# Optimization experiments

Measured on AMD Instinct MI355X. Metric: run time of the kernel, lower is better.

## Reference

```python
import jax, jax.numpy as jnp
import numpy as np

B, T, E, A = 512, 64, 1024, 32
S, D, H = 30, 200, 200          # stoch, deter, hidden
SS = D + S                      # state_size = 230
MIN_STD = 0.1
UPDATE_BIAS = -1.0
W_SCALE = 0.05


def setup_inputs() -> dict:
    key = jax.random.key(0)
    ks = jax.random.split(key, 17)
    n = jax.random.normal
    return {
        "embed":       n(ks[0], (B, T, E), jnp.float32),
        "action":      n(ks[1], (B, T, A), jnp.float32),
        "context":     n(ks[2], (B, T, SS), jnp.float32),
        "noise_prior": n(ks[3], (T, B, S), jnp.float32),
        "noise_post":  n(ks[4], (T, B, S), jnp.float32),
        "w_inp":       n(ks[5], (S + SS + A, H), jnp.float32) * W_SCALE,
        "b_inp":       jnp.zeros((H,), jnp.float32),
        "w_gru":       n(ks[6], (H + D, 3 * D), jnp.float32) * W_SCALE,
        "b_gru":       jnp.zeros((3 * D,), jnp.float32),
        "w_img_out":   n(ks[7], (D, H), jnp.float32) * W_SCALE,
        "b_img_out":   jnp.zeros((H,), jnp.float32),
        "w_obs_out":   n(ks[8], (D + E, H), jnp.float32) * W_SCALE,
        "b_obs_out":   jnp.zeros((H,), jnp.float32),
        "w_ims_stat":  n(ks[9], (H, 2 * S), jnp.float32) * W_SCALE,
        "b_ims_stat":  jnp.zeros((2 * S,), jnp.float32),
        "w_obs_stat":  n(ks[10], (H, 2 * S), jnp.float32) * W_SCALE,
        "b_obs_stat":  jnp.zeros((2 * S,), jnp.float32),
    }


def _observe(embed, action, context, noise_prior, noise_post,
             w_inp, b_inp, w_gru, b_gru, w_img_out, b_img_out,
             w_obs_out, b_obs_out, w_ims_stat, b_ims_stat,
             w_obs_stat, b_obs_stat):
    # time-major
    emb_t = jnp.swapaxes(embed, 0, 1)    # [T,B,E]
    act_t = jnp.swapaxes(action, 0, 1)   # [T,B,A]
    ctx_t = jnp.swapaxes(context, 0, 1)  # [T,B,SS]

    def step(carry, xs):
        stoch, deter = carry
        ctx, act, emb, n_p, n_o = xs
        # img_step: input MLP + GRU cell
        x = jnp.concatenate([stoch, ctx, act], -1)
        x = jax.nn.elu(x @ w_inp + b_inp)
        parts = jnp.concatenate([x, deter], -1) @ w_gru + b_gru
        reset, cand, update = jnp.split(parts, 3, -1)
        reset = jax.nn.sigmoid(reset)
        cand = jnp.tanh(reset * cand)
        update = jax.nn.sigmoid(update + UPDATE_BIAS)
        deter_new = update * cand + (1.0 - update) * deter
        # prior stats
        h = jax.nn.elu(deter_new @ w_img_out + b_img_out)
        st = h @ w_ims_stat + b_ims_stat
        pm, ps = jnp.split(st, 2, -1)
        ps = jax.nn.softplus(ps) + MIN_STD
        p_stoch = pm + ps * n_p
        # posterior stats
        ho = jax.nn.elu(jnp.concatenate([deter_new, emb], -1) @ w_obs_out + b_obs_out)
        so = ho @ w_obs_stat + b_obs_stat
        om, os_ = jnp.split(so, 2, -1)
        os_ = jax.nn.softplus(os_) + MIN_STD
        o_stoch = om + os_ * n_o
        out = jnp.concatenate([om, os_, o_stoch, pm, ps, p_stoch, deter_new], -1)
        return (o_stoch, deter_new), out

    carry0 = (jnp.zeros((B, S), embed.dtype), jnp.zeros((B, D), embed.dtype))
    _, ys = jax.lax.scan(step, carry0, (ctx_t, act_t, emb_t, noise_prior, noise_post))
    # ys: [T,B,6S+D] -> [B,T,6S+D]  (post mean/std/stoch, prior mean/std/stoch, deter)
    return jnp.swapaxes(ys, 0, 1)


def reference(embed, action, context, noise_prior, noise_post,
              w_inp, b_inp, w_gru, b_gru, w_img_out, b_img_out,
              w_obs_out, b_obs_out, w_ims_stat, b_ims_stat,
              w_obs_stat, b_obs_stat):
    return _observe(embed, action, context, noise_prior, noise_post,
                    w_inp, b_inp, w_gru, b_gru, w_img_out, b_img_out,
                    w_obs_out, b_obs_out, w_ims_stat, b_ims_stat,
                    w_obs_stat, b_obs_stat)
```

## Files before the change

### kernel.cpp

```cpp
#include <hip/hip_runtime.h>
#include <cstddef>

typedef short short8 __attribute__((ext_vector_type(8)));
typedef float f32x4 __attribute__((ext_vector_type(4)));
typedef unsigned short u16;

#define Bn 512
#define Tn 64
#define En 1024
#define An 32
#define Sn 30
#define Dn 200
#define SSn 230
#define OUTC 380

#define U16_WINP0  0
#define U16_WINPCA 6656
#define U16_WGRU   66560
#define U16_WIMG   326144
#define U16_WOBSD  372736
#define U16_WIMS   419328
#define U16_WOBSS  433664
#define U16_WOBSE  448000
#define U16_PREO   660992
#define U16_PREI   7214592

#define WINP0_8  0
#define WINPCA_8 832
#define WGRU_8   8320
#define WIMG_8   40768
#define WOBSD_8  46592
#define WIMS_8   52416
#define WOBSS_8  54208
#define WOBSE_8  56000

#define DEV static __device__ __forceinline__
#define MFMA(a,b,c) __builtin_amdgcn_mfma_f32_16x16x32_bf16((a),(b),(c),0,0,0)

DEV u16 f2bf(float f) {
  union { float f; unsigned u; } v; v.f = f;
  return (u16)((v.u + 0x7FFFu + ((v.u >> 16) & 1u)) >> 16);
}
DEV float bf2f(u16 h) {
  union { unsigned u; float f; } v; v.u = ((unsigned)h) << 16; return v.f;
}
DEV float fexp(float x)  { return __builtin_amdgcn_exp2f(x * 1.44269504f); }
DEV float sigm(float x)  { return __builtin_amdgcn_rcpf(1.f + fexp(-x)); }
DEV float tanhf_(float x){ return 1.f - 2.f * __builtin_amdgcn_rcpf(fexp(2.f * x) + 1.f); }
DEV float elu1(float x)  { return x > 0.f ? x : fexp(x) - 1.f; }
DEV float splus(float x) { return 0.69314718f * __builtin_amdgcn_logf(1.f + fexp(x)); }

DEV void barx() {
  asm volatile("s_waitcnt lgkmcnt(0)" ::: "memory");
  __builtin_amdgcn_s_barrier();
  asm volatile("" ::: "memory");
}

__global__ __launch_bounds__(256) void k_pack2(
    const float* __restrict__ w_inp, const float* __restrict__ w_gru,
    const float* __restrict__ w_img, const float* __restrict__ w_obs,
    const float* __restrict__ w_ims, const float* __restrict__ w_obss,
    u16* __restrict__ ws) {
  int s = blockIdx.x;
  const float* src; int KT, Kr, ldN, roff, colbase, cmax; size_t dstbase; int ntKT;
  if (s < 13)      { src=w_inp;  KT=1;  Kr=30;   ldN=200; roff=0;   int nt=s;    colbase=nt*16; cmax=min(16,200-colbase); dstbase=U16_WINP0;  ntKT=nt*KT; }
  else if (s < 26) { src=w_inp;  KT=9;  Kr=262;  ldN=200; roff=30;  int nt=s-13; colbase=nt*16; cmax=min(16,200-colbase); dstbase=U16_WINPCA; ntKT=nt*KT; }
  else if (s < 65) { src=w_gru;  KT=13; Kr=400;  ldN=600; roff=0;   int ntp=s-26; int g=ntp/3, p=ntp%3;
                     colbase=p*200+g*16; cmax=min(16,200-g*16); dstbase=U16_WGRU; ntKT=ntp*KT; }
  else if (s < 78) { src=w_img;  KT=7;  Kr=200;  ldN=200; roff=0;   int nt=s-65; colbase=nt*16; cmax=min(16,200-colbase); dstbase=U16_WIMG;  ntKT=nt*KT; }
  else if (s < 91) { src=w_obs;  KT=7;  Kr=200;  ldN=200; roff=0;   int nt=s-78; colbase=nt*16; cmax=min(16,200-colbase); dstbase=U16_WOBSD; ntKT=nt*KT; }
  else if (s < 95) { src=w_ims;  KT=7;  Kr=200;  ldN=60;  roff=0;   int nt=s-91; colbase=nt*16; cmax=min(16,60-colbase);  dstbase=U16_WIMS;  ntKT=nt*KT; }
  else if (s < 99) { src=w_obss; KT=7;  Kr=200;  ldN=60;  roff=0;   int nt=s-95; colbase=nt*16; cmax=min(16,60-colbase);  dstbase=U16_WOBSS; ntKT=nt*KT; }
  else             { src=w_obs;  KT=32; Kr=1024; ldN=200; roff=200; int nt=s-99; colbase=nt*16; cmax=min(16,200-colbase); dstbase=U16_WOBSE; ntKT=nt*KT; }

  __shared__ float Ws[2048];
  int tid = threadIdx.x;
  int nchunk = (KT + 3) >> 2;
  for (int kc = 0; kc < nchunk; ++kc) {
    __syncthreads();
    for (int i = tid; i < 2048; i += 256) {
      int r = i >> 4, c = i & 15;
      int k = kc * 128 + r;
      Ws[i] = (k < Kr && c < cmax) ? src[(size_t)(roff + k) * ldN + colbase + c] : 0.f;
    }
    __syncthreads();
    int nf = KT - kc * 4; if (nf > 4) nf = 4;
    int fi = tid >> 6, lane = tid & 63;
    if (fi < nf) {
      int kt = kc * 4 + fi;
      union { u16 h[8]; short8 v; } pk;
#pragma unroll
      for (int j = 0; j < 8; ++j)
        pk.h[j] = f2bf(Ws[(fi * 32 + ((lane >> 4) << 3) + j) * 16 + (lane & 15)]);
      *(short8*)&ws[dstbase + (size_t)(ntKT + kt) * 512 + lane * 8] = pk.v;
    }
  }
}

__global__ __launch_bounds__(256) void k_pre(
    const float* __restrict__ emb, const float* __restrict__ ctx,
    const float* __restrict__ act, const float* __restrict__ b_obs,
    const float* __restrict__ b_inp, u16* __restrict__ ws) {
  __shared__ u16 Asm[64 * 72];
  __shared__ short8 Bsm[26 * 64];
  const short8* Wb = (const short8*)ws;
  u16* preO = ws + U16_PREO;
  u16* preI = ws + U16_PREI;

  int tid = threadIdx.x, wv = tid >> 6, lane = tid & 63;
  int lrow = lane & 15, quad = lane >> 4;
  int m0 = blockIdx.x * 64;
  int t = m0 >> 9, b0 = m0 & 511;

  const f32x4 z4 = {0.f, 0.f, 0.f, 0.f};
  f32x4 acc[13];

#pragma unroll
  for (int i = 0; i < 13; ++i) acc[i] = z4;
  for (int kc = 0; kc < 16; ++kc) {
    __syncthreads();
#pragma unroll
    for (int q = 0; q < 4; ++q) {
      int i = tid + q * 256;
      int row = i >> 4, c4 = i & 15;
      const float* src = emb + ((size_t)((b0 + row) * Tn + t)) * En + kc * 64 + c4 * 4;
      float4 v = *(const float4*)src;
      union { u16 h[4]; unsigned long long ll; } p;
      p.h[0] = f2bf(v.x); p.h[1] = f2bf(v.y); p.h[2] = f2bf(v.z); p.h[3] = f2bf(v.w);
      *(unsigned long long*)&Asm[row * 72 + c4 * 4] = p.ll;
    }
    for (int q = 0; q < 7; ++q) {
      int i = tid + q * 256;
      if (i < 1664) {
        int pair = i >> 6, l = i & 63;
        int ktl = pair / 13, nt = pair % 13;
        Bsm[i] = Wb[WOBSE_8 + (size_t)(nt * 32 + kc * 2 + ktl) * 64 + l];
      }
    }
    __syncthreads();
#pragma unroll
    for (int ktl = 0; ktl < 2; ++ktl) {
      short8 a = *(const short8*)&Asm[(wv * 16 + lrow) * 72 + ktl * 32 + quad * 8];
#pragma unroll
      for (int nt = 0; nt < 13; ++nt)
        acc[nt] = MFMA(a, Bsm[(ktl * 13 + nt) * 64 + lane], acc[nt]);
    }
  }
#pragma unroll
  for (int nt = 0; nt < 13; ++nt) {
    int col = nt * 16 + lrow;
    if (col < 200) {
      float bias = b_obs[col];
#pragma unroll
      for (int r = 0; r < 4; ++r) {
        int m = t * 512 + b0 + wv * 16 + quad * 4 + r;
        preO[(size_t)m * 200 + col] = f2bf(acc[nt][r] + bias);
      }
    }
  }

#pragma unroll
  for (int i = 0; i < 13; ++i) acc[i] = z4;
  for (int kc = 0; kc < 5; ++kc) {
    __syncthreads();
#pragma unroll
    for (int q = 0; q < 4; ++q) {
      int i = tid + q * 256;
      int row = i >> 4, c4 = i & 15;
      union { u16 h[4]; unsigned long long ll; } p;
#pragma unroll
      for (int e = 0; e < 4; ++e) {
        int k = kc * 64 + c4 * 4 + e;
        float v = 0.f;
        if (k < 230)      v = ctx[((size_t)(b0 + row) * Tn + t) * SSn + k];
        else if (k < 262) v = act[((size_t)(b0 + row) * Tn + t) * An + (k - 230)];
        p.h[e] = f2bf(v);
      }
      *(unsigned long long*)&Asm[row * 72 + c4 * 4] = p.ll;
    }
    int nktl = (kc < 4) ? 2 : 1;
    for (int q = 0; q < 7; ++q) {
      int i = tid + q * 256;
      if (i < nktl * 13 * 64) {
        int pair = i >> 6, l = i & 63;
        int ktl = pair / 13, nt = pair % 13;
        Bsm[i] = Wb[WINPCA_8 + (size_t)(nt * 9 + kc * 2 + ktl) * 64 + l];
      }
    }
    __syncthreads();
    for (int ktl = 0; ktl < nktl; ++ktl) {
      short8 a = *(const short8*)&Asm[(wv * 16 + lrow) * 72 + ktl * 32 + quad * 8];
#pragma unroll
      for (int nt = 0; nt < 13; ++nt)
        acc[nt] = MFMA(a, Bsm[(ktl * 13 + nt) * 64 + lane], acc[nt]);
    }
  }
#pragma unroll
  for (int nt = 0; nt < 13; ++nt) {
    int col = nt * 16 + lrow;
    if (col < 200) {
      float bias = b_inp[col];
#pragma unroll
      for (int r = 0; r < 4; ++r) {
        int m = t * 512 + b0 + wv * 16 + quad * 4 + r;
        preI[(size_t)m * 200 + col] = f2bf(acc[nt][r] + bias);
      }
    }
  }
}

__global__ __launch_bounds__(512, 1) void k_scan(
    const float* __restrict__ g_no, const float* __restrict__ b_gru,
    const float* __restrict__ b_obss, const u16* __restrict__ ws,
    float* __restrict__ out) {

  __shared__ u16 AB[16 * 872];
  __shared__ u16 Uin[16 * 40];
  __shared__ u16 hoA[16 * 232];
  __shared__ u16 WdL[91 * 512];

  const short8* Wb = (const short8*)ws;
  const u16* preO = ws + U16_PREO;
  const u16* preI = ws + U16_PREI;

  const int tid = threadIdx.x, wv = tid >> 6, lane = tid & 63;
  const int lrow = lane & 15, quad = lane >> 4;
  const int b0 = blockIdx.x * 16;
  const f32x4 z4 = {0.f, 0.f, 0.f, 0.f};

  const bool two = wv < 5;
  const int g1 = two ? (wv + 8) : wv;
  const int colA0 = wv * 16 + lrow;
  const int colA1 = g1 * 16 + lrow;
  const int dcol0 = colA0;
  const int dcol1 = colA1;
  const int nrow = tid / 30, ns = tid - nrow * 30;

  short8 fA0 = Wb[WINP0_8 + (size_t)wv * 64 + lane];
  short8 fA1 = Wb[WINP0_8 + (size_t)g1 * 64 + lane];

  float bgr0 = b_gru[dcol0], bgc0 = b_gru[200 + dcol0], bgu0 = b_gru[400 + dcol0] - 1.f;
  float bgr1 = 0.f, bgc1 = 0.f, bgu1 = -1.f;
  if (two && dcol1 < 200) { bgr1 = b_gru[dcol1]; bgc1 = b_gru[200 + dcol1]; bgu1 = b_gru[400 + dcol1] - 1.f; }
  const int cD = (wv & 3) * 16 + lrow;
  const float bD = (wv < 4 && cD < 60) ? b_obss[cD] : 0.f;

  const short8* pr0 = Wb + WGRU_8 + (size_t)((3 * wv + 0) * 13) * 64 + lane;
  const short8* pc0 = Wb + WGRU_8 + (size_t)((3 * wv + 1) * 13) * 64 + lane;
  const short8* pu0 = Wb + WGRU_8 + (size_t)((3 * wv + 2) * 13) * 64 + lane;
  const short8* pr1 = Wb + WGRU_8 + (size_t)((3 * g1 + 0) * 13) * 64 + lane;
  const short8* pc1 = Wb + WGRU_8 + (size_t)((3 * g1 + 1) * 13) * 64 + lane;
  const short8* pu1 = Wb + WGRU_8 + (size_t)((3 * g1 + 2) * 13) * 64 + lane;
  const short8* bpD = Wb + WOBSS_8 + (size_t)(((wv < 4) ? wv : 0) * 7) * 64 + lane;

  short8 wR0[2], wC0_[2], wU0[2], wR1[2], wC1_[2], wU1[2];
#pragma unroll
  for (int k = 0; k < 2; ++k) {
    wR0[k] = pr0[k * 64]; wC0_[k] = pc0[k * 64]; wU0[k] = pu0[k * 64];
    wR1[k] = pr1[k * 64]; wC1_[k] = pc1[k * 64]; wU1[k] = pu1[k * 64];
  }
  short8 wD[7];
#pragma unroll
  for (int k = 0; k < 7; ++k) wD[k] = bpD[k * 64];

  {
    short8* Wl = (short8*)WdL;
    for (int i = tid; i < 91 * 64; i += 512) Wl[i] = Wb[WOBSD_8 + i];
  }

  for (int i = tid; i < 16 * 872; i += 512) AB[i] = 0;
  for (int i = tid; i < 16 * 40; i += 512) Uin[i] = 0;
  for (int i = tid; i < 16 * 232; i += 512) hoA[i] = 0;
  __syncthreads();

  float* stoF = (float*)AB;

  u16 pinC0[4], pinC1[4] = {0,0,0,0}, pobC0[4], pobC1[4] = {0,0,0,0};
  float vnoC = 0.f;
  {
    size_t mb = (size_t)b0 + quad * 4;
#pragma unroll
    for (int r = 0; r < 4; ++r) pinC0[r] = preI[(mb + r) * 200 + colA0];
#pragma unroll
    for (int r = 0; r < 4; ++r) pobC0[r] = preO[(mb + r) * 200 + colA0];
    if (two && colA1 < 200) {
#pragma unroll
      for (int r = 0; r < 4; ++r) pinC1[r] = preI[(mb + r) * 200 + colA1];
#pragma unroll
      for (int r = 0; r < 4; ++r) pobC1[r] = preO[(mb + r) * 200 + colA1];
    }
    if (tid < 480) vnoC = g_no[((size_t)b0 + nrow) * Sn + ns];
  }

  for (int t = 0; t < Tn; ++t) {
    const int par = t & 1;
    const int pb = par * 424, qb = 424 - pb;
    const int qbf = qb >> 1;

    barx();

    {
      short8 aU = *(const short8*)&Uin[lrow * 40 + quad * 8];
      f32x4 a0 = MFMA(aU, fA0, z4);
#pragma unroll
      for (int r = 0; r < 4; ++r)
        AB[(quad * 4 + r) * 872 + pb + colA0] = f2bf(elu1(a0[r] + bf2f(pinC0[r])));
      if (two) {
        f32x4 a1 = MFMA(aU, fA1, z4);
        if (colA1 < 200) {
#pragma unroll
          for (int r = 0; r < 4; ++r)
            AB[(quad * 4 + r) * 872 + pb + colA1] = f2bf(elu1(a1[r] + bf2f(pinC1[r])));
        }
      }
    }

    u16 pinN0[4], pinN1[4] = {0,0,0,0}, pobN0[4], pobN1[4] = {0,0,0,0};
    float vnoN = 0.f;
    {
      int tn = (t + 1 < Tn) ? (t + 1) : t;
      size_t mb = (size_t)tn * 512 + b0 + quad * 4;
#pragma unroll
      for (int r = 0; r < 4; ++r) pinN0[r] = preI[(mb + r) * 200 + colA0];
#pragma unroll
      for (int r = 0; r < 4; ++r) pobN0[r] = preO[(mb + r) * 200 + colA0];
      if (two && colA1 < 200) {
#pragma unroll
        for (int r = 0; r < 4; ++r) pinN1[r] = preI[(mb + r) * 200 + colA1];
#pragma unroll
        for (int r = 0; r < 4; ++r) pobN1[r] = preO[(mb + r) * 200 + colA1];
      }
      if (tid < 480) vnoN = g_no[((size_t)tn * 512 + b0 + nrow) * Sn + ns];
    }

    barx();

    {
      short8 ax[13];
#pragma unroll
      for (int kt = 0; kt < 13; ++kt)
        ax[kt] = *(const short8*)&AB[lrow * 872 + pb + kt * 32 + quad * 8];
      f32x4 ar0 = z4, ac0 = z4, au0 = z4, ar1 = z4, ac1 = z4, au1 = z4;
      if (two) {
#pragma unroll
        for (int kt = 0; kt < 13; ++kt) {
          short8 br0 = (kt < 2) ? wR0[kt]  : pr0[kt * 64];
          short8 br1 = (kt < 2) ? wR1[kt]  : pr1[kt * 64];
          short8 bc0 = (kt < 2) ? wC0_[kt] : pc0[kt * 64];
          short8 bc1 = (kt < 2) ? wC1_[kt] : pc1[kt * 64];
          short8 bu0 = (kt < 2) ? wU0[kt]  : pu0[kt * 64];
          short8 bu1 = (kt < 2) ? wU1[kt]  : pu1[kt * 64];
          ar0 = MFMA(ax[kt], br0, ar0);
          ar1 = MFMA(ax[kt], br1, ar1);
          ac0 = MFMA(ax[kt], bc0, ac0);
          ac1 = MFMA(ax[kt], bc1, ac1);
          au0 = MFMA(ax[kt], bu0, au0);
          au1 = MFMA(ax[kt], bu1, au1);
        }
      } else {
#pragma unroll
        for (int kt = 0; kt < 13; ++kt) {
          short8 br0 = (kt < 2) ? wR0[kt]  : pr0[kt * 64];
          short8 bc0 = (kt < 2) ? wC0_[kt] : pc0[kt * 64];
          short8 bu0 = (kt < 2) ? wU0[kt]  : pu0[kt * 64];
          ar0 = MFMA(ax[kt], br0, ar0);
          ac0 = MFMA(ax[kt], bc0, ac0);
          au0 = MFMA(ax[kt], bu0, au0);
        }
      }
#pragma unroll
      for (int r = 0; r < 4; ++r) {
        int row = quad * 4 + r;
        float dold = bf2f(AB[row * 872 + pb + 200 + dcol0]);
        float rs = sigm(ar0[r] + bgr0);
        float cnd = tanhf_(rs * (ac0[r] + bgc0));
        float up = sigm(au0[r] + bgu0);
        float dn = up * cnd + (1.f - up) * dold;
        AB[row * 872 + qb + 200 + dcol0] = f2bf(dn);
        __builtin_nontemporal_store(dn, &out[((size_t)(b0 + row) * Tn + t) * OUTC + 180 + dcol0]);
      }
      if (two && dcol1 < 200) {
#pragma unroll
        for (int r = 0; r < 4; ++r) {
          int row = quad * 4 + r;
          float dold = bf2f(AB[row * 872 + pb + 200 + dcol1]);
          float rs = sigm(ar1[r] + bgr1);
          float cnd = tanhf_(rs * (ac1[r] + bgc1));
          float up = sigm(au1[r] + bgu1);
          float dn = up * cnd + (1.f - up) * dold;
          AB[row * 872 + qb + 200 + dcol1] = f2bf(dn);
          __builtin_nontemporal_store(dn, &out[((size_t)(b0 + row) * Tn + t) * OUTC + 180 + dcol1]);
        }
      }
    }

    barx();

    {
      short8 ad[7];
#pragma unroll
      for (int kt = 0; kt < 7; ++kt)
        ad[kt] = *(const short8*)&AB[lrow * 872 + qb + 200 + kt * 32 + quad * 8];
      f32x4 h0 = z4, h1 = z4;
      if (two) {
#pragma unroll
        for (int kt = 0; kt < 7; ++kt) {
          h0 = MFMA(ad[kt], *(const short8*)&WdL[(wv * 7 + kt) * 512 + lane * 8], h0);
          h1 = MFMA(ad[kt], *(const short8*)&WdL[(g1 * 7 + kt) * 512 + lane * 8], h1);
        }
      } else {
#pragma unroll
        for (int kt = 0; kt < 7; ++kt)
          h0 = MFMA(ad[kt], *(const short8*)&WdL[(wv * 7 + kt) * 512 + lane * 8], h0);
      }
#pragma unroll
      for (int r = 0; r < 4; ++r)
        hoA[(quad * 4 + r) * 232 + colA0] = f2bf(elu1(h0[r] + bf2f(pobC0[r])));
      if (two && colA1 < 200) {
#pragma unroll
        for (int r = 0; r < 4; ++r)
          hoA[(quad * 4 + r) * 232 + colA1] = f2bf(elu1(h1[r] + bf2f(pobC1[r])));
      }
    }

    barx();

    if (wv < 4) {
      f32x4 acc = z4;
#pragma unroll
      for (int kt = 0; kt < 7; ++kt) {
        short8 a = *(const short8*)&hoA[lrow * 232 + kt * 32 + quad * 8];
        acc = MFMA(a, wD[kt], acc);
      }
      if (cD < 60) {
#pragma unroll
        for (int r = 0; r < 4; ++r)
          stoF[(quad * 4 + r) * 436 + qbf + cD] = acc[r] + bD;
      }
    }

    barx();

    if (tid < 480) {
      size_t ob = ((size_t)(b0 + nrow) * Tn + t) * OUTC;
      float om = stoF[nrow * 436 + qbf + ns];
      float os = splus(stoF[nrow * 436 + qbf + 30 + ns]) + 0.1f;
      float ost = om + os * vnoC;
      __builtin_nontemporal_store(om,  &out[ob + ns]);
      __builtin_nontemporal_store(os,  &out[ob + 30 + ns]);
      __builtin_nontemporal_store(ost, &out[ob + 60 + ns]);
      Uin[nrow * 40 + ns] = f2bf(ost);
    }

#pragma unroll
    for (int r = 0; r < 4; ++r) {
      pinC0[r] = pinN0[r]; pinC1[r] = pinN1[r];
      pobC0[r] = pobN0[r]; pobC1[r] = pobN1[r];
    }
    vnoC = vnoN;
  }
}

__global__ __launch_bounds__(256) void k_prior(
    const float* __restrict__ g_np, const float* __restrict__ b_img,
    const float* __restrict__ b_ims, const u16* __restrict__ ws,
    float* __restrict__ out) {
  __shared__ u16 Ad[64 * 232];
  __shared__ u16 Ah[64 * 232];
  __shared__ float stf[64 * 66];
  const short8* Wb = (const short8*)ws;

  int tid = threadIdx.x, wv = tid >> 6, lane = tid & 63;
  int lrow = lane & 15, quad = lane >> 4;
  int b = blockIdx.x;
  const f32x4 z4 = {0.f, 0.f, 0.f, 0.f};

  for (int i = tid; i < 64 * 232; i += 256) { Ad[i] = 0; Ah[i] = 0; }
  __syncthreads();

  for (int idx = tid; idx < 64 * 200; idx += 256) {
    int row = idx / 200, col = idx - row * 200;
    Ad[row * 232 + col] = f2bf(out[((size_t)b * Tn + row) * OUTC + 180 + col]);
  }
  __syncthreads();

  {
    short8 af[7];
#pragma unroll
    for (int kt = 0; kt < 7; ++kt)
      af[kt] = *(const short8*)&Ad[(wv * 16 + lrow) * 232 + kt * 32 + quad * 8];
    for (int nt = 0; nt < 13; ++nt) {
      const short8* bp = Wb + WIMG_8 + (size_t)(nt * 7) * 64 + lane;
      f32x4 acc = z4;
#pragma unroll
      for (int kt = 0; kt < 7; ++kt) acc = MFMA(af[kt], bp[kt * 64], acc);
      int col = nt * 16 + lrow;
      if (col < 200) {
        float bias = b_img[col];
#pragma unroll
        for (int r = 0; r < 4; ++r)
          Ah[(wv * 16 + quad * 4 + r) * 232 + col] = f2bf(elu1(acc[r] + bias));
      }
    }
  }
  __syncthreads();

  {
    short8 ah[7];
#pragma unroll
    for (int kt = 0; kt < 7; ++kt)
      ah[kt] = *(const short8*)&Ah[(wv * 16 + lrow) * 232 + kt * 32 + quad * 8];
#pragma unroll
    for (int nt = 0; nt < 4; ++nt) {
      const short8* bp = Wb + WIMS_8 + (size_t)(nt * 7) * 64 + lane;
      f32x4 acc = z4;
#pragma unroll
      for (int kt = 0; kt < 7; ++kt) acc = MFMA(ah[kt], bp[kt * 64], acc);
      int col = nt * 16 + lrow;
      if (col < 60) {
        float bias = b_ims[col];
#pragma unroll
        for (int r = 0; r < 4; ++r)
          stf[(wv * 16 + quad * 4 + r) * 66 + col] = acc[r] + bias;
      }
    }
  }
  __syncthreads();

  for (int idx = tid; idx < 64 * 30; idx += 256) {
    int row = idx / 30, s = idx - row * 30;
    float pm = stf[row * 66 + s];
    float ps = splus(stf[row * 66 + 30 + s]) + 0.1f;
    float pst = pm + ps * g_np[((size_t)row * 512 + b) * Sn + s];
    size_t ob = ((size_t)b * Tn + row) * OUTC;
    __builtin_nontemporal_store(pm,  &out[ob + 90 + s]);
    __builtin_nontemporal_store(ps,  &out[ob + 120 + s]);
    __builtin_nontemporal_store(pst, &out[ob + 150 + s]);
  }
}

extern "C" void kernel_launch(void* const* d_in, const int* in_sizes, int n_in,
                              void* d_out, int out_size, void* d_ws, size_t ws_size,
                              hipStream_t stream) {
  (void)in_sizes; (void)n_in; (void)out_size; (void)ws_size;
  const float* emb    = (const float*)d_in[0];
  const float* action = (const float*)d_in[1];
  const float* ctx    = (const float*)d_in[2];
  const float* np_    = (const float*)d_in[3];
  const float* no_    = (const float*)d_in[4];
  const float* w_inp  = (const float*)d_in[5];
  const float* b_inp  = (const float*)d_in[6];
  const float* w_gru  = (const float*)d_in[7];
  const float* b_gru  = (const float*)d_in[8];
  const float* w_img  = (const float*)d_in[9];
  const float* b_img  = (const float*)d_in[10];
  const float* w_obs  = (const float*)d_in[11];
  const float* b_obs  = (const float*)d_in[12];
  const float* w_ims  = (const float*)d_in[13];
  const float* b_ims  = (const float*)d_in[14];
  const float* w_obss = (const float*)d_in[15];
  const float* b_obss = (const float*)d_in[16];

  u16* wsu = (u16*)d_ws;
  float* out = (float*)d_out;

  k_pack2<<<112, 256, 0, stream>>>(w_inp, w_gru, w_img, w_obs, w_ims, w_obss, wsu);
  k_pre<<<512, 256, 0, stream>>>(emb, ctx, action, b_obs, b_inp, wsu);
  k_scan<<<32, 512, 0, stream>>>(no_, b_gru, b_obss, wsu, out);
  k_prior<<<512, 256, 0, stream>>>(np_, b_img, b_ims, wsu, out);
}
```

Before: 1.248 ms.

## Add writer warps to scan kernel to offload global output stores

The scan kernel grows from 8 to 10 waves. The two extra waves take over the global output stores (deter and posterior stats), the noise prefetch, and the softplus/sampling epilogue, while the 8 compute waves stage deter values in a new shared buffer. Compute waves no longer issue global stores on the serial recurrence path, and the register-cached first GRU weight tiles are dropped. The cost is more threads per block, more shared memory and extra LDS traffic. The epilogue is now spread over only 128 threads instead of 480, which may lengthen that serial phase.

```diff
diff --git a/kernel.cpp b/kernel.cpp
--- a/kernel.cpp
+++ b/kernel.cpp
@@ -209,7 +209,7 @@
   }
 }
 
-__global__ __launch_bounds__(512, 1) void k_scan(
+__global__ __launch_bounds__(640, 1) void k_scan(
     const float* __restrict__ g_no, const float* __restrict__ b_gru,
     const float* __restrict__ b_obss, const u16* __restrict__ ws,
     float* __restrict__ out) {
@@ -218,6 +218,7 @@
   __shared__ u16 Uin[16 * 40];
   __shared__ u16 hoA[16 * 232];
   __shared__ u16 WdL[91 * 512];
+  __shared__ float detF[16 * 200];
 
   const short8* Wb = (const short8*)ws;
   const u16* preO = ws + U16_PREO;
@@ -227,57 +228,54 @@
   const int lrow = lane & 15, quad = lane >> 4;
   const int b0 = blockIdx.x * 16;
   const f32x4 z4 = {0.f, 0.f, 0.f, 0.f};
+  const bool comp = wv < 8;
+  const int wtid = tid - 512;
 
   const bool two = wv < 5;
-  const int g1 = two ? (wv + 8) : wv;
+  const int g1 = (comp && two) ? (wv + 8) : wv;
   const int colA0 = wv * 16 + lrow;
   const int colA1 = g1 * 16 + lrow;
   const int dcol0 = colA0;
   const int dcol1 = colA1;
-  const int nrow = tid / 30, ns = tid - nrow * 30;
-
-  short8 fA0 = Wb[WINP0_8 + (size_t)wv * 64 + lane];
-  short8 fA1 = Wb[WINP0_8 + (size_t)g1 * 64 + lane];
-
-  float bgr0 = b_gru[dcol0], bgc0 = b_gru[200 + dcol0], bgu0 = b_gru[400 + dcol0] - 1.f;
+
+  const int wvc = comp ? wv : 0;
+  short8 fA0 = Wb[WINP0_8 + (size_t)wvc * 64 + lane];
+  short8 fA1 = Wb[WINP0_8 + (size_t)(comp ? g1 : 0) * 64 + lane];
+
+  const int dc0s = comp ? dcol0 : 0;
+  float bgr0 = b_gru[dc0s], bgc0 = b_gru[200 + dc0s], bgu0 = b_gru[400 + dc0s] - 1.f;
   float bgr1 = 0.f, bgc1 = 0.f, bgu1 = -1.f;
-  if (two && dcol1 < 200) { bgr1 = b_gru[dcol1]; bgc1 = b_gru[200 + dcol1]; bgu1 = b_gru[400 + dcol1] - 1.f; }
+  if (comp && two && dcol1 < 200) { bgr1 = b_gru[dcol1]; bgc1 = b_gru[200 + dcol1]; bgu1 = b_gru[400 + dcol1] - 1.f; }
   const int cD = (wv & 3) * 16 + lrow;
-  const float bD = (wv < 4 && cD < 60) ? b_obss[cD] : 0.f;
-
-  const short8* pr0 = Wb + WGRU_8 + (size_t)((3 * wv + 0) * 13) * 64 + lane;
-  const short8* pc0 = Wb + WGRU_8 + (size_t)((3 * wv + 1) * 13) * 64 + lane;
-  const short8* pu0 = Wb + WGRU_8 + (size_t)((3 * wv + 2) * 13) * 64 + lane;
+  const float bD = (comp && wv < 4 && cD < 60) ? b_obss[cD] : 0.f;
+
+  const short8* pr0 = Wb + WGRU_8 + (size_t)((3 * wvc + 0) * 13) * 64 + lane;
+  const short8* pc0 = Wb + WGRU_8 + (size_t)((3 * wvc + 1) * 13) * 64 + lane;
+  const short8* pu0 = Wb + WGRU_8 + (size_t)((3 * wvc + 2) * 13) * 64 + lane;
   const short8* pr1 = Wb + WGRU_8 + (size_t)((3 * g1 + 0) * 13) * 64 + lane;
   const short8* pc1 = Wb + WGRU_8 + (size_t)((3 * g1 + 1) * 13) * 64 + lane;
   const short8* pu1 = Wb + WGRU_8 + (size_t)((3 * g1 + 2) * 13) * 64 + lane;
-  const short8* bpD = Wb + WOBSS_8 + (size_t)(((wv < 4) ? wv : 0) * 7) * 64 + lane;
-
-  short8 wR0[2], wC0_[2], wU0[2], wR1[2], wC1_[2], wU1[2];
-#pragma unroll
-  for (int k = 0; k < 2; ++k) {
-    wR0[k] = pr0[k * 64]; wC0_[k] = pc0[k * 64]; wU0[k] = pu0[k * 64];
-    wR1[k] = pr1[k * 64]; wC1_[k] = pc1[k * 64]; wU1[k] = pu1[k * 64];
-  }
+  const short8* bpD = Wb + WOBSS_8 + (size_t)(((comp && wv < 4) ? wv : 0) * 7) * 64 + lane;
+
   short8 wD[7];
 #pragma unroll
   for (int k = 0; k < 7; ++k) wD[k] = bpD[k * 64];
 
   {
     short8* Wl = (short8*)WdL;
-    for (int i = tid; i < 91 * 64; i += 512) Wl[i] = Wb[WOBSD_8 + i];
-  }
-
-  for (int i = tid; i < 16 * 872; i += 512) AB[i] = 0;
-  for (int i = tid; i < 16 * 40; i += 512) Uin[i] = 0;
-  for (int i = tid; i < 16 * 232; i += 512) hoA[i] = 0;
+    for (int i = tid; i < 91 * 64; i += 640) Wl[i] = Wb[WOBSD_8 + i];
+  }
+
+  for (int i = tid; i < 16 * 872; i += 640) AB[i] = 0;
+  for (int i = tid; i < 16 * 40; i += 640) Uin[i] = 0;
+  for (int i = tid; i < 16 * 232; i += 640) hoA[i] = 0;
   __syncthreads();
 
   float* stoF = (float*)AB;
 
   u16 pinC0[4], pinC1[4] = {0,0,0,0}, pobC0[4], pobC1[4] = {0,0,0,0};
-  float vnoC = 0.f;
-  {
+  float vnoW[4] = {0.f,0.f,0.f,0.f};
+  if (comp) {
     size_t mb = (size_t)b0 + quad * 4;
 #pragma unroll
     for (int r = 0; r < 4; ++r) pinC0[r] = preI[(mb + r) * 200 + colA0];
@@ -289,7 +287,12 @@
 #pragma unroll
       for (int r = 0; r < 4; ++r) pobC1[r] = preO[(mb + r) * 200 + colA1];
     }
-    if (tid < 480) vnoC = g_no[((size_t)b0 + nrow) * Sn + ns];
+  } else {
+#pragma unroll
+    for (int k = 0; k < 4; ++k) {
+      int item = wtid + k * 128;
+      if (item < 480) vnoW[k] = g_no[((size_t)b0 + item / 30) * Sn + item % 30];
+    }
   }
 
   for (int t = 0; t < Tn; ++t) {
@@ -299,7 +302,10 @@
 
     barx();
 
-    {
+    u16 pinN0[4], pinN1[4] = {0,0,0,0}, pobN0[4], pobN1[4] = {0,0,0,0};
+    float vnoN[4] = {0.f,0.f,0.f,0.f};
+
+    if (comp) {
       short8 aU = *(const short8*)&Uin[lrow * 40 + quad * 8];
       f32x4 a0 = MFMA(aU, fA0, z4);
 #pragma unroll
@@ -313,11 +319,6 @@
             AB[(quad * 4 + r) * 872 + pb + colA1] = f2bf(elu1(a1[r] + bf2f(pinC1[r])));
         }
       }
-    }
-
-    u16 pinN0[4], pinN1[4] = {0,0,0,0}, pobN0[4], pobN1[4] = {0,0,0,0};
-    float vnoN = 0.f;
-    {
       int tn = (t + 1 < Tn) ? (t + 1) : t;
       size_t mb = (size_t)tn * 512 + b0 + quad * 4;
 #pragma unroll
@@ -330,12 +331,18 @@
 #pragma unroll
         for (int r = 0; r < 4; ++r) pobN1[r] = preO[(mb + r) * 200 + colA1];
       }
-      if (tid < 480) vnoN = g_no[((size_t)tn * 512 + b0 + nrow) * Sn + ns];
+    } else {
+      int tn = (t + 1 < Tn) ? (t + 1) : t;
+#pragma unroll
+      for (int k = 0; k < 4; ++k) {
+        int item = wtid + k * 128;
+        if (item < 480) vnoN[k] = g_no[((size_t)tn * 512 + b0 + item / 30) * Sn + item % 30];
+      }
     }
 
     barx();
 
-    {
+    if (comp) {
       short8 ax[13];
 #pragma unroll
       for (int kt = 0; kt < 13; ++kt)
@@ -344,28 +351,19 @@
       if (two) {
 #pragma unroll
         for (int kt = 0; kt < 13; ++kt) {
-          short8 br0 = (kt < 2) ? wR0[kt]  : pr0[kt * 64];
-          short8 br1 = (kt < 2) ? wR1[kt]  : pr1[kt * 64];
-          short8 bc0 = (kt < 2) ? wC0_[kt] : pc0[kt * 64];
-          short8 bc1 = (kt < 2) ? wC1_[kt] : pc1[kt * 64];
-          short8 bu0 = (kt < 2) ? wU0[kt]  : pu0[kt * 64];
-          short8 bu1 = (kt < 2) ? wU1[kt]  : pu1[kt * 64];
-          ar0 = MFMA(ax[kt], br0, ar0);
-          ar1 = MFMA(ax[kt], br1, ar1);
-          ac0 = MFMA(ax[kt], bc0, ac0);
-          ac1 = MFMA(ax[kt], bc1, ac1);
-          au0 = MFMA(ax[kt], bu0, au0);
-          au1 = MFMA(ax[kt], bu1, au1);
+          ar0 = MFMA(ax[kt], pr0[kt * 64], ar0);
+          ar1 = MFMA(ax[kt], pr1[kt * 64], ar1);
+          ac0 = MFMA(ax[kt], pc0[kt * 64], ac0);
+          ac1 = MFMA(ax[kt], pc1[kt * 64], ac1);
+          au0 = MFMA(ax[kt], pu0[kt * 64], au0);
+          au1 = MFMA(ax[kt], pu1[kt * 64], au1);
         }
       } else {
 #pragma unroll
         for (int kt = 0; kt < 13; ++kt) {
-          short8 br0 = (kt < 2) ? wR0[kt]  : pr0[kt * 64];
-          short8 bc0 = (kt < 2) ? wC0_[kt] : pc0[kt * 64];
-          short8 bu0 = (kt < 2) ? wU0[kt]  : pu0[kt * 64];
-          ar0 = MFMA(ax[kt], br0, ar0);
-          ac0 = MFMA(ax[kt], bc0, ac0);
-          au0 = MFMA(ax[kt], bu0, au0);
+          ar0 = MFMA(ax[kt], pr0[kt * 64], ar0);
+          ac0 = MFMA(ax[kt], pc0[kt * 64], ac0);
+          au0 = MFMA(ax[kt], pu0[kt * 64], au0);
         }
       }
 #pragma unroll
@@ -377,7 +375,7 @@
         float up = sigm(au0[r] + bgu0);
         float dn = up * cnd + (1.f - up) * dold;
         AB[row * 872 + qb + 200 + dcol0] = f2bf(dn);
-        __builtin_nontemporal_store(dn, &out[((size_t)(b0 + row) * Tn + t) * OUTC + 180 + dcol0]);
+        detF[row * 200 + dcol0] = dn;
       }
       if (two && dcol1 < 200) {
 #pragma unroll
@@ -389,14 +387,14 @@
           float up = sigm(au1[r] + bgu1);
           float dn = up * cnd + (1.f - up) * dold;
           AB[row * 872 + qb + 200 + dcol1] = f2bf(dn);
-          __builtin_nontemporal_store(dn, &out[((size_t)(b0 + row) * Tn + t) * OUTC + 180 + dcol1]);
+          detF[row * 200 + dcol1] = dn;
         }
       }
     }
 
     barx();
 
-    {
+    if (comp) {
       short8 ad[7];
 #pragma unroll
       for (int kt = 0; kt < 7; ++kt)
@@ -421,11 +419,19 @@
         for (int r = 0; r < 4; ++r)
           hoA[(quad * 4 + r) * 232 + colA1] = f2bf(elu1(h1[r] + bf2f(pobC1[r])));
       }
+    } else {
+#pragma unroll
+      for (int k = 0; k < 25; ++k) {
+        int item = wtid + k * 128;
+        int row = item / 200, col = item - row * 200;
+        float dn = detF[row * 200 + col];
+        __builtin_nontemporal_store(dn, &out[((size_t)(b0 + row) * Tn + t) * OUTC + 180 + col]);
+      }
     }
 
     barx();
 
-    if (wv < 4) {
+    if (comp && wv < 4) {
       f32x4 acc = z4;
 #pragma unroll
       for (int kt = 0; kt < 7; ++kt) {
@@ -441,23 +447,34 @@
 
     barx();
 
-    if (tid < 480) {
-      size_t ob = ((size_t)(b0 + nrow) * Tn + t) * OUTC;
-      float om = stoF[nrow * 436 + qbf + ns];
-      float os = splus(stoF[nrow * 436 + qbf + 30 + ns]) + 0.1f;
-      float ost = om + os * vnoC;
-      __builtin_nontemporal_store(om,  &out[ob + ns]);
-      __builtin_nontemporal_store(os,  &out[ob + 30 + ns]);
-      __builtin_nontemporal_store(ost, &out[ob + 60 + ns]);
-      Uin[nrow * 40 + ns] = f2bf(ost);
-    }
-
-#pragma unroll
-    for (int r = 0; r < 4; ++r) {
-      pinC0[r] = pinN0[r]; pinC1[r] = pinN1[r];
-      pobC0[r] = pobN0[r]; pobC1[r] = pobN1[r];
-    }
-    vnoC = vnoN;
+    if (!comp) {
+#pragma unroll
+      for (int k = 0; k < 4; ++k) {
+        int item = wtid + k * 128;
+        if (item < 480) {
+          int nrow = item / 30, ns = item - nrow * 30;
+          size_t ob = ((size_t)(b0 + nrow) * Tn + t) * OUTC;
+          float om = stoF[nrow * 436 + qbf + ns];
+          float os = splus(stoF[nrow * 436 + qbf + 30 + ns]) + 0.1f;
+          float ost = om + os * vnoW[k];
+          __builtin_nontemporal_store(om,  &out[ob + ns]);
+          __builtin_nontemporal_store(os,  &out[ob + 30 + ns]);
+          __builtin_nontemporal_store(ost, &out[ob + 60 + ns]);
+          Uin[nrow * 40 + ns] = f2bf(ost);
+        }
+      }
+    }
+
+    if (comp) {
+#pragma unroll
+      for (int r = 0; r < 4; ++r) {
+        pinC0[r] = pinN0[r]; pinC1[r] = pinN1[r];
+        pobC0[r] = pobN0[r]; pobC1[r] = pobN1[r];
+      }
+    } else {
+#pragma unroll
+      for (int k = 0; k < 4; ++k) vnoW[k] = vnoN[k];
+    }
   }
 }
 
@@ -566,6 +583,6 @@
 
   k_pack2<<<112, 256, 0, stream>>>(w_inp, w_gru, w_img, w_obs, w_ims, w_obss, wsu);
   k_pre<<<512, 256, 0, stream>>>(emb, ctx, action, b_obs, b_inp, wsu);
-  k_scan<<<32, 512, 0, stream>>>(no_, b_gru, b_obss, wsu, out);
+  k_scan<<<32, 640, 0, stream>>>(no_, b_gru, b_obss, wsu, out);
   k_prior<<<512, 256, 0, stream>>>(np_, b_img, b_ims, wsu, out);
 }
```

Measured after the change: 1.839 ms. 1.47x slower.
